# Optimization experiments

Hardware: AMD Instinct MI355X
Metric: run time of the kernel (lower is better)

Reference implementation:

```python
import jax, jax.numpy as jnp
import numpy as np
from jax.scipy.linalg import expm

DELTA = 0.01  # time step from __init__ delta
B_SZ, U_DIM, DU_DIM, H_DIM, Y_DIM = 512, 1024, 512, 2048, 1024


def setup_inputs() -> dict:
    key = jax.random.key(0)
    ks = jax.random.split(key, 6)
    inv_sqrt = lambda fan_in: 1.0 / np.sqrt(fan_in)
    u = jax.random.normal(ks[0], (B_SZ, U_DIM), jnp.float32)
    du = jax.random.normal(ks[1], (B_SZ, DU_DIM), jnp.float32)
    # torch.nn.Linear default init: U(-1/sqrt(fan_in), 1/sqrt(fan_in))
    W = jax.random.uniform(ks[2], (H_DIM, H_DIM), jnp.float32, -inv_sqrt(H_DIM), inv_sqrt(H_DIM))
    Bw = jax.random.uniform(ks[3], (H_DIM, U_DIM + DU_DIM), jnp.float32, -inv_sqrt(U_DIM + DU_DIM), inv_sqrt(U_DIM + DU_DIM))
    Cw = jax.random.uniform(ks[4], (Y_DIM, H_DIM), jnp.float32, -inv_sqrt(H_DIM), inv_sqrt(H_DIM))
    h = jax.random.normal(ks[5], (1, H_DIM), jnp.float32)
    return {"u": u, "du": du, "W": W, "Bw": Bw, "Cw": Cw, "h": h}


def reference(u, du, W, Bw, Cw, h):
    # Antisymmetric part of W
    A = 0.5 * (W - W.T)                                    # (H,H)
    A_expm = expm(A * DELTA)                               # (H,H) matrix exponential
    rec = h @ A_expm.T                                     # (1,H) recurrent term: F.linear(h, A_expm)
    A_inv = jnp.linalg.inv(A)                              # (H,H)
    # B(cat([du, u])) : (B, H)
    b = jnp.concatenate([du, u], axis=1) @ Bw.T
    # M = A^{-1} (expm(A*delta) - I); input term = M @ b^T per sample -> b @ M^T
    M = A_inv @ (A_expm - jnp.eye(H_DIM, dtype=A.dtype))   # (H,H)
    inp = b @ M.T                                          # (B,H)
    h_new = rec + inp                                      # broadcast (1,H)+(B,H) -> (B,H)
    y = h_new @ Cw.T                                       # (B,Y)
    return y
```

## Files before the change

### kernel.cpp

```cpp
#include <hip/hip_runtime.h>
#include <hip/hip_bf16.h>


#define B_SZ 512
#define U_DIM 1024
#define DU_DIM 512
#define H_DIM 2048
#define Y_DIM 1024
#define K_CAT 1536
#define DELTA_F 0.01f

typedef __hip_bfloat16 bf16;
using bf16x8f = __attribute__((ext_vector_type(8))) short;
using f32x4   = __attribute__((ext_vector_type(4))) float;

__device__ __forceinline__ short f2bs(float x) {
  union { bf16 b; short s; } u; u.b = __float2bfloat16(x); return u.s;
}
__device__ __forceinline__ int4 pack8(const float4 v0, const float4 v1) {
  union { short s[8]; int4 i; } o;
  o.s[0] = f2bs(v0.x); o.s[1] = f2bs(v0.y); o.s[2] = f2bs(v0.z); o.s[3] = f2bs(v0.w);
  o.s[4] = f2bs(v1.x); o.s[5] = f2bs(v1.y); o.s[6] = f2bs(v1.z); o.s[7] = f2bs(v1.w);
  return o.i;
}

#define LDP 72
#define LDS_SHORTS (2 * 32 * LDP + 2 * 64 * LDP)

__device__ __forceinline__ void bb_tile(short* lds, const float* __restrict__ du,
                                        const float* __restrict__ u, const float* __restrict__ Bw,
                                        short* __restrict__ bb, int mt, int nt) {
  const int KDIM = K_CAT;
  short* As0 = lds;
  short* Bs0 = lds + 2 * 32 * LDP;
  const int tid = threadIdx.x;
  const int lane = tid & 63, wave = tid >> 6;
  const int wm = wave >> 1, wn = wave & 1;
  const int row0 = mt * 32, col0 = nt * 64;
  const int rA = tid >> 3, kc = (tid & 7) * 8;
  f32x4 acc[2] = {};
  int4 pa, pb1, pb2;
  auto ldA = [&](int kt) -> int4 {
    int col = kt * 64 + kc;
    const float* p = (col < DU_DIM) ? du + (size_t)(row0 + rA) * DU_DIM + col
                                    : u + (size_t)(row0 + rA) * U_DIM + (col - DU_DIM);
    return pack8(*(const float4*)p, *(const float4*)(p + 4));
  };
  auto ldB1 = [&](int kt) -> int4 {
    const float* p = Bw + (size_t)(col0 + rA) * KDIM + kt * 64 + kc;
    return pack8(*(const float4*)p, *(const float4*)(p + 4));
  };
  auto ldB2 = [&](int kt) -> int4 {
    const float* p = Bw + (size_t)(col0 + rA + 32) * KDIM + kt * 64 + kc;
    return pack8(*(const float4*)p, *(const float4*)(p + 4));
  };
  pa = ldA(0); pb1 = ldB1(0); pb2 = ldB2(0);
  *(int4*)&As0[rA * LDP + kc] = pa;
  *(int4*)&Bs0[rA * LDP + kc] = pb1;
  *(int4*)&Bs0[(rA + 32) * LDP + kc] = pb2;
  const int NT = KDIM / 64;
  const int kq = (lane >> 4) * 8, rm = lane & 15;
  for (int kt = 0; kt < NT; kt++) {
    const int cur = kt & 1;
    if (kt + 1 < NT) { pa = ldA(kt + 1); pb1 = ldB1(kt + 1); pb2 = ldB2(kt + 1); }
    __syncthreads();
    const short* Ac = As0 + cur * (32 * LDP);
    const short* Bc = Bs0 + cur * (64 * LDP);
    bf16x8f af[2], bfr[2][2];
#pragma unroll
    for (int ks = 0; ks < 2; ks++) {
      af[ks] = *(const bf16x8f*)&Ac[(wm * 16 + rm) * LDP + ks * 32 + kq];
#pragma unroll
      for (int j = 0; j < 2; j++)
        bfr[ks][j] = *(const bf16x8f*)&Bc[(wn * 32 + 16 * j + rm) * LDP + ks * 32 + kq];
    }
#pragma unroll
    for (int ks = 0; ks < 2; ks++)
#pragma unroll
      for (int j = 0; j < 2; j++)
        acc[j] = __builtin_amdgcn_mfma_f32_16x16x32_bf16(af[ks], bfr[ks][j], acc[j], 0, 0, 0);
    if (kt + 1 < NT) {
      short* An = As0 + (cur ^ 1) * (32 * LDP);
      short* Bn = Bs0 + (cur ^ 1) * (64 * LDP);
      *(int4*)&An[rA * LDP + kc] = pa;
      *(int4*)&Bn[rA * LDP + kc] = pb1;
      *(int4*)&Bn[(rA + 32) * LDP + kc] = pb2;
      __syncthreads();
    }
  }
  const int quad = lane >> 4;
#pragma unroll
  for (int j = 0; j < 2; j++) {
    int gc = col0 + wn * 32 + 16 * j + rm;
#pragma unroll
    for (int r = 0; r < 4; r++) {
      int gr = row0 + wm * 16 + quad * 4 + r;
      bb[(size_t)gr * H_DIM + gc] = f2bs(DELTA_F * acc[j][r]);
    }
  }
}

__global__ __launch_bounds__(256) void kA(const float* __restrict__ du, const float* __restrict__ u,
                                          const float* __restrict__ Bw, const float* __restrict__ W,
                                          const float* __restrict__ h, short* __restrict__ bb,
                                          float* __restrict__ wh, float* __restrict__ wtp) {
  __shared__ __align__(16) short lds[LDS_SHORTS];
  const int b = blockIdx.x;
  if ((b & 1) == 0) {
    const int t = b >> 1;
    bb_tile(lds, du, u, Bw, bb, t >> 5, t & 31);
  } else {
    const int e = b >> 1;
    if (e < 256) {
      const int lane = threadIdx.x & 63, wave = threadIdx.x >> 6;
#pragma unroll
      for (int i = 0; i < 2; i++) {
        const int row = e * 8 + wave * 2 + i;
        const float* wr = W + (size_t)row * H_DIM;
        float s = 0.f;
#pragma unroll
        for (int it = 0; it < 8; it++) {
          int k = it * 256 + lane * 4;
          float4 a = *(const float4*)(wr + k);
          float4 hv = *(const float4*)(h + k);
          s += a.x * hv.x + a.y * hv.y + a.z * hv.z + a.w * hv.w;
        }
#pragma unroll
        for (int off = 32; off > 0; off >>= 1) s += __shfl_down(s, off);
        if (lane == 0) wh[row] = s;
      }
    } else {
      const int e2 = e - 256;
      const int colg = e2 & 7, rowg = e2 >> 3;
      const int k = colg * 256 + threadIdx.x;
      float s = 0.f;
      const float* base = W + (size_t)rowg * 64 * H_DIM + k;
#pragma unroll 8
      for (int i = 0; i < 64; i++) s += base[(size_t)i * H_DIM] * h[rowg * 64 + i];
      wtp[rowg * H_DIM + k] = s;
    }
  }
}

__global__ __launch_bounds__(256) void kB(const float* __restrict__ Cw, const float* __restrict__ h,
                                          const float* __restrict__ wh, const float* __restrict__ wtp,
                                          float* __restrict__ yrec) {
  __shared__ float recs[H_DIM];
  const int tid = threadIdx.x;
  {
    const int k0 = tid * 8;
    float s[8] = {};
#pragma unroll 8
    for (int p = 0; p < 32; p++) {
      float4 w0 = *(const float4*)(wtp + p * H_DIM + k0);
      float4 w1 = *(const float4*)(wtp + p * H_DIM + k0 + 4);
      s[0] += w0.x; s[1] += w0.y; s[2] += w0.z; s[3] += w0.w;
      s[4] += w1.x; s[5] += w1.y; s[6] += w1.z; s[7] += w1.w;
    }
    float4 h0 = *(const float4*)(h + k0);
    float4 h1 = *(const float4*)(h + k0 + 4);
    float4 a0 = *(const float4*)(wh + k0);
    float4 a1 = *(const float4*)(wh + k0 + 4);
    recs[k0 + 0] = h0.x + 0.005f * (a0.x - s[0]);
    recs[k0 + 1] = h0.y + 0.005f * (a0.y - s[1]);
    recs[k0 + 2] = h0.z + 0.005f * (a0.z - s[2]);
    recs[k0 + 3] = h0.w + 0.005f * (a0.w - s[3]);
    recs[k0 + 4] = h1.x + 0.005f * (a1.x - s[4]);
    recs[k0 + 5] = h1.y + 0.005f * (a1.y - s[5]);
    recs[k0 + 6] = h1.z + 0.005f * (a1.z - s[6]);
    recs[k0 + 7] = h1.w + 0.005f * (a1.w - s[7]);
  }
  __syncthreads();
  const int lane = tid & 63, wave = tid >> 6;
  const int row = blockIdx.x * 4 + wave;
  const float* cr = Cw + (size_t)row * H_DIM;
  float s = 0.f;
#pragma unroll
  for (int it = 0; it < 8; it++) {
    int k = it * 256 + lane * 4;
    float4 c = *(const float4*)(cr + k);
    float4 r = *(const float4*)(recs + k);
    s += c.x * r.x + c.y * r.y + c.z * r.z + c.w * r.w;
  }
#pragma unroll
  for (int off = 32; off > 0; off >>= 1) s += __shfl_down(s, off);
  if (lane == 0) yrec[row] = s;
}

__global__ __launch_bounds__(256) void kC(const short* __restrict__ bb, const float* __restrict__ Cw,
                                          const float* __restrict__ yrec, float* __restrict__ y) {
  __shared__ __align__(16) short lds[LDS_SHORTS];
  const int KDIM = H_DIM;
  short* As0 = lds;
  short* Bs0 = lds + 2 * 32 * LDP;
  const int tid = threadIdx.x;
  const int lane = tid & 63, wave = tid >> 6;
  const int wm = wave >> 1, wn = wave & 1;
  const int mt = blockIdx.x >> 5, nt = blockIdx.x & 31;
  const int row0 = mt * 32, col0 = nt * 32;
  const int rA = tid >> 3, kc = (tid & 7) * 8;
  f32x4 acc = {};
  int4 pa, pb;
  auto ldA = [&](int kt) { return *(const int4*)(bb + (size_t)(row0 + rA) * KDIM + kt * 64 + kc); };
  auto ldB = [&](int kt) -> int4 {
    const float* p = Cw + (size_t)(col0 + rA) * KDIM + kt * 64 + kc;
    return pack8(*(const float4*)p, *(const float4*)(p + 4));
  };
  pa = ldA(0); pb = ldB(0);
  *(int4*)&As0[rA * LDP + kc] = pa;
  *(int4*)&Bs0[rA * LDP + kc] = pb;
  const int NT = KDIM / 64;
  const int kq = (lane >> 4) * 8, rm = lane & 15;
  for (int kt = 0; kt < NT; kt++) {
    const int cur = kt & 1;
    if (kt + 1 < NT) { pa = ldA(kt + 1); pb = ldB(kt + 1); }
    __syncthreads();
    const short* Ac = As0 + cur * (32 * LDP);
    const short* Bc = Bs0 + cur * (32 * LDP);
#pragma unroll
    for (int ks = 0; ks < 2; ks++) {
      bf16x8f af = *(const bf16x8f*)&Ac[(wm * 16 + rm) * LDP + ks * 32 + kq];
      bf16x8f bf = *(const bf16x8f*)&Bc[(wn * 16 + rm) * LDP + ks * 32 + kq];
      acc = __builtin_amdgcn_mfma_f32_16x16x32_bf16(af, bf, acc, 0, 0, 0);
    }
    if (kt + 1 < NT) {
      short* An = As0 + (cur ^ 1) * (32 * LDP);
      short* Bn = Bs0 + (cur ^ 1) * (32 * LDP);
      *(int4*)&An[rA * LDP + kc] = pa;
      *(int4*)&Bn[rA * LDP + kc] = pb;
      __syncthreads();
    }
  }
  const int quad = lane >> 4;
  int gc = col0 + wn * 16 + rm;
#pragma unroll
  for (int r = 0; r < 4; r++) {
    int gr = row0 + wm * 16 + quad * 4 + r;
    y[(size_t)gr * Y_DIM + gc] = yrec[gc] + acc[r];
  }
}

extern "C" void kernel_launch(void* const* d_in, const int* in_sizes, int n_in,
                              void* d_out, int out_size, void* d_ws, size_t ws_size,
                              hipStream_t stream) {
  const float* u  = (const float*)d_in[0];
  const float* du = (const float*)d_in[1];
  const float* W  = (const float*)d_in[2];
  const float* Bw = (const float*)d_in[3];
  const float* Cw = (const float*)d_in[4];
  const float* h  = (const float*)d_in[5];
  float* y = (float*)d_out;

  char* w = (char*)d_ws;
  size_t off = 0;
  short* bb  = (short*)(w + off); off += (size_t)B_SZ * H_DIM * sizeof(short);
  float* wh  = (float*)(w + off); off += H_DIM * sizeof(float);
  float* wtp = (float*)(w + off); off += 32 * H_DIM * sizeof(float);
  float* yrec= (float*)(w + off); off += Y_DIM * sizeof(float);
  if (ws_size < off) return;

  kA<<<1024, 256, 0, stream>>>(du, u, Bw, W, h, bb, wh, wtp);
  kB<<<Y_DIM / 4, 256, 0, stream>>>(Cw, h, wh, wtp, yrec);
  kC<<<512, 256, 0, stream>>>(bb, Cw, yrec, y);
}
```

Baseline: 134.1 us.

## Fuse recurrent-term GEMV into output GEMM and drop middle kernel

The separate kernel that reduced W^T h partials and computed the Cw·rec vector is removed. The W^T h column sums are now fully reduced inside the first kernel using row-strided float4 loads and a shuffle/LDS reduction. Each output-GEMM block rebuilds rec in shared memory and computes its 32 Cw·rec dot products from the Cw values it already loads for the MFMA B operand. This saves one launch and the partial-sum traffic, but every one of the 512 blocks now redundantly builds the 2048-element rec vector and does extra FMAs inside the load path.

```diff
diff --git a/kernel.cpp b/kernel.cpp
--- a/kernel.cpp
+++ b/kernel.cpp
@@ -25,7 +25,8 @@
 }
 
 #define LDP 72
-#define LDS_SHORTS (2 * 32 * LDP + 2 * 64 * LDP)
+#define LDS_A64B (2 * 32 * LDP + 2 * 64 * LDP)
+#define LDS_A32B (2 * 32 * LDP + 2 * 32 * LDP)
 
 __device__ __forceinline__ void bb_tile(short* lds, const float* __restrict__ du,
                                         const float* __restrict__ u, const float* __restrict__ Bw,
@@ -100,19 +101,21 @@
   }
 }
 
-__global__ __launch_bounds__(256) void kA(const float* __restrict__ du, const float* __restrict__ u,
+__global__ __launch_bounds__(256) void k1(const float* __restrict__ du, const float* __restrict__ u,
                                           const float* __restrict__ Bw, const float* __restrict__ W,
                                           const float* __restrict__ h, short* __restrict__ bb,
-                                          float* __restrict__ wh, float* __restrict__ wtp) {
-  __shared__ __align__(16) short lds[LDS_SHORTS];
+                                          float* __restrict__ wh, float* __restrict__ wth) {
+  __shared__ __align__(16) short lds[LDS_A64B];
+  __shared__ float red[4][8];
   const int b = blockIdx.x;
   if ((b & 1) == 0) {
     const int t = b >> 1;
     bb_tile(lds, du, u, Bw, bb, t >> 5, t & 31);
   } else {
     const int e = b >> 1;
+    const int tid = threadIdx.x;
     if (e < 256) {
-      const int lane = threadIdx.x & 63, wave = threadIdx.x >> 6;
+      const int lane = tid & 63, wave = tid >> 6;
 #pragma unroll
       for (int i = 0; i < 2; i++) {
         const int row = e * 8 + wave * 2 + i;
@@ -130,66 +133,38 @@
         if (lane == 0) wh[row] = s;
       }
     } else {
-      const int e2 = e - 256;
-      const int colg = e2 & 7, rowg = e2 >> 3;
-      const int k = colg * 256 + threadIdx.x;
-      float s = 0.f;
-      const float* base = W + (size_t)rowg * 64 * H_DIM + k;
-#pragma unroll 8
-      for (int i = 0; i < 64; i++) s += base[(size_t)i * H_DIM] * h[rowg * 64 + i];
-      wtp[rowg * H_DIM + k] = s;
-    }
-  }
-}
-
-__global__ __launch_bounds__(256) void kB(const float* __restrict__ Cw, const float* __restrict__ h,
-                                          const float* __restrict__ wh, const float* __restrict__ wtp,
-                                          float* __restrict__ yrec) {
+      const int k0 = (e - 256) * 8;
+      float s[8] = {};
+#pragma unroll
+      for (int i = 0; i < 8; i++) {
+        const int r = tid + 256 * i;
+        const float* p = W + (size_t)r * H_DIM + k0;
+        float4 w0 = *(const float4*)p;
+        float4 w1 = *(const float4*)(p + 4);
+        float hv = h[r];
+        s[0] += w0.x * hv; s[1] += w0.y * hv; s[2] += w0.z * hv; s[3] += w0.w * hv;
+        s[4] += w1.x * hv; s[5] += w1.y * hv; s[6] += w1.z * hv; s[7] += w1.w * hv;
+      }
+      const int lane = tid & 63, wave = tid >> 6;
+#pragma unroll
+      for (int c = 0; c < 8; c++) {
+        float v = s[c];
+#pragma unroll
+        for (int off = 32; off > 0; off >>= 1) v += __shfl_down(v, off);
+        if (lane == 0) red[wave][c] = v;
+      }
+      __syncthreads();
+      if (tid < 8) wth[k0 + tid] = red[0][tid] + red[1][tid] + red[2][tid] + red[3][tid];
+    }
+  }
+}
+
+__global__ __launch_bounds__(256) void k2(const short* __restrict__ bb, const float* __restrict__ Cw,
+                                          const float* __restrict__ h, const float* __restrict__ wh,
+                                          const float* __restrict__ wth, float* __restrict__ y) {
+  __shared__ __align__(16) short lds[LDS_A32B];
   __shared__ float recs[H_DIM];
-  const int tid = threadIdx.x;
-  {
-    const int k0 = tid * 8;
-    float s[8] = {};
-#pragma unroll 8
-    for (int p = 0; p < 32; p++) {
-      float4 w0 = *(const float4*)(wtp + p * H_DIM + k0);
-      float4 w1 = *(const float4*)(wtp + p * H_DIM + k0 + 4);
-      s[0] += w0.x; s[1] += w0.y; s[2] += w0.z; s[3] += w0.w;
-      s[4] += w1.x; s[5] += w1.y; s[6] += w1.z; s[7] += w1.w;
-    }
-    float4 h0 = *(const float4*)(h + k0);
-    float4 h1 = *(const float4*)(h + k0 + 4);
-    float4 a0 = *(const float4*)(wh + k0);
-    float4 a1 = *(const float4*)(wh + k0 + 4);
-    recs[k0 + 0] = h0.x + 0.005f * (a0.x - s[0]);
-    recs[k0 + 1] = h0.y + 0.005f * (a0.y - s[1]);
-    recs[k0 + 2] = h0.z + 0.005f * (a0.z - s[2]);
-    recs[k0 + 3] = h0.w + 0.005f * (a0.w - s[3]);
-    recs[k0 + 4] = h1.x + 0.005f * (a1.x - s[4]);
-    recs[k0 + 5] = h1.y + 0.005f * (a1.y - s[5]);
-    recs[k0 + 6] = h1.z + 0.005f * (a1.z - s[6]);
-    recs[k0 + 7] = h1.w + 0.005f * (a1.w - s[7]);
-  }
-  __syncthreads();
-  const int lane = tid & 63, wave = tid >> 6;
-  const int row = blockIdx.x * 4 + wave;
-  const float* cr = Cw + (size_t)row * H_DIM;
-  float s = 0.f;
-#pragma unroll
-  for (int it = 0; it < 8; it++) {
-    int k = it * 256 + lane * 4;
-    float4 c = *(const float4*)(cr + k);
-    float4 r = *(const float4*)(recs + k);
-    s += c.x * r.x + c.y * r.y + c.z * r.z + c.w * r.w;
-  }
-#pragma unroll
-  for (int off = 32; off > 0; off >>= 1) s += __shfl_down(s, off);
-  if (lane == 0) yrec[row] = s;
-}
-
-__global__ __launch_bounds__(256) void kC(const short* __restrict__ bb, const float* __restrict__ Cw,
-                                          const float* __restrict__ yrec, float* __restrict__ y) {
-  __shared__ __align__(16) short lds[LDS_SHORTS];
+  __shared__ float yrecs[32];
   const int KDIM = H_DIM;
   short* As0 = lds;
   short* Bs0 = lds + 2 * 32 * LDP;
@@ -199,12 +174,33 @@
   const int mt = blockIdx.x >> 5, nt = blockIdx.x & 31;
   const int row0 = mt * 32, col0 = nt * 32;
   const int rA = tid >> 3, kc = (tid & 7) * 8;
+  {
+    const int k0 = tid * 8;
+    float4 h0 = *(const float4*)(h + k0),   h1 = *(const float4*)(h + k0 + 4);
+    float4 a0 = *(const float4*)(wh + k0),  a1 = *(const float4*)(wh + k0 + 4);
+    float4 b0 = *(const float4*)(wth + k0), b1 = *(const float4*)(wth + k0 + 4);
+    recs[k0 + 0] = h0.x + 0.005f * (a0.x - b0.x);
+    recs[k0 + 1] = h0.y + 0.005f * (a0.y - b0.y);
+    recs[k0 + 2] = h0.z + 0.005f * (a0.z - b0.z);
+    recs[k0 + 3] = h0.w + 0.005f * (a0.w - b0.w);
+    recs[k0 + 4] = h1.x + 0.005f * (a1.x - b1.x);
+    recs[k0 + 5] = h1.y + 0.005f * (a1.y - b1.y);
+    recs[k0 + 6] = h1.z + 0.005f * (a1.z - b1.z);
+    recs[k0 + 7] = h1.w + 0.005f * (a1.w - b1.w);
+  }
+  __syncthreads();
   f32x4 acc = {};
+  float dotacc = 0.f;
   int4 pa, pb;
   auto ldA = [&](int kt) { return *(const int4*)(bb + (size_t)(row0 + rA) * KDIM + kt * 64 + kc); };
   auto ldB = [&](int kt) -> int4 {
     const float* p = Cw + (size_t)(col0 + rA) * KDIM + kt * 64 + kc;
-    return pack8(*(const float4*)p, *(const float4*)(p + 4));
+    float4 v0 = *(const float4*)p;
+    float4 v1 = *(const float4*)(p + 4);
+    const float* rp = recs + kt * 64 + kc;
+    dotacc += v0.x * rp[0] + v0.y * rp[1] + v0.z * rp[2] + v0.w * rp[3]
+            + v1.x * rp[4] + v1.y * rp[5] + v1.z * rp[6] + v1.w * rp[7];
+    return pack8(v0, v1);
   };
   pa = ldA(0); pb = ldB(0);
   *(int4*)&As0[rA * LDP + kc] = pa;
@@ -231,12 +227,16 @@
       __syncthreads();
     }
   }
+#pragma unroll
+  for (int off = 4; off > 0; off >>= 1) dotacc += __shfl_down(dotacc, off, 8);
+  if ((tid & 7) == 0) yrecs[rA] = dotacc;
+  __syncthreads();
   const int quad = lane >> 4;
   int gc = col0 + wn * 16 + rm;
 #pragma unroll
   for (int r = 0; r < 4; r++) {
     int gr = row0 + wm * 16 + quad * 4 + r;
-    y[(size_t)gr * Y_DIM + gc] = yrec[gc] + acc[r];
+    y[(size_t)gr * Y_DIM + gc] = yrecs[gc - col0] + acc[r];
   }
 }
 
@@ -255,11 +255,9 @@
   size_t off = 0;
   short* bb  = (short*)(w + off); off += (size_t)B_SZ * H_DIM * sizeof(short);
   float* wh  = (float*)(w + off); off += H_DIM * sizeof(float);
-  float* wtp = (float*)(w + off); off += 32 * H_DIM * sizeof(float);
-  float* yrec= (float*)(w + off); off += Y_DIM * sizeof(float);
+  float* wth = (float*)(w + off); off += H_DIM * sizeof(float);
   if (ws_size < off) return;
 
-  kA<<<1024, 256, 0, stream>>>(du, u, Bw, W, h, bb, wh, wtp);
-  kB<<<Y_DIM / 4, 256, 0, stream>>>(Cw, h, wh, wtp, yrec);
-  kC<<<512, 256, 0, stream>>>(bb, Cw, yrec, y);
-}
+  k1<<<1024, 256, 0, stream>>>(du, u, Bw, W, h, bb, wh, wth);
+  k2<<<512, 256, 0, stream>>>(bb, Cw, h, wh, wth, y);
+}
```

Measured after the change: 129.6 us. 1.03x faster.
